# Kernel tuning notes

Measured on AMD Instinct MI355X. Metric: run time of the kernel, lower is better.

## Reference

```python
import jax, jax.numpy as jnp
import numpy as np

G, MAXN, NPG, EPG = 2048, 30, 24, 288   # graphs, dense pad size, real nodes/graph, edges/graph
K, EMB, DH, ATOM_TYPES = 32, 32, 64, 10  # gaussian basis, embed_dim, cfg.gt.dim_hidden, atom types


def setup_inputs() -> dict:
    key = jax.random.key(0)
    ks = jax.random.split(key, 12)
    N = G * NPG
    E = G * EPG
    z = jax.random.randint(ks[0], (N,), 1, ATOM_TYPES).astype(jnp.int32)  # 1..9; 0 = padding idx
    pos = jax.random.normal(ks[1], (N, 3), jnp.float32) * 3.0
    batch_mapping = (jnp.arange(N) // NPG).astype(jnp.int32)
    # radius-graph style edges, endpoints within the same graph (global node ids)
    gidx = jnp.arange(E) // EPG
    src_local = jax.random.randint(ks[2], (E,), 0, NPG)
    dst_local = jax.random.randint(ks[3], (E,), 0, NPG)
    edge_index = jnp.stack([gidx * NPG + src_local, gidx * NPG + dst_local]).astype(jnp.int32)
    atom_emb = (jax.random.normal(ks[4], (ATOM_TYPES, EMB), jnp.float32) * 0.02).at[0].set(0.0)
    W_edge_proj = jax.random.normal(ks[5], (K, EMB), jnp.float32) / np.sqrt(K)
    b_edge_proj = jnp.zeros((EMB,), jnp.float32)
    gbf_means = jax.random.uniform(ks[6], (K,), jnp.float32, minval=0.0, maxval=3.0)
    gbf_stds = jax.random.uniform(ks[7], (K,), jnp.float32, minval=0.1, maxval=2.0)
    gbf_mul = jax.random.normal(ks[8], (ATOM_TYPES * ATOM_TYPES,), jnp.float32)
    gbf_bias = jax.random.normal(ks[9], (ATOM_TYPES * ATOM_TYPES,), jnp.float32)
    W_nodes = jax.random.normal(ks[10], (EMB, DH), jnp.float32) / np.sqrt(EMB)
    b_nodes = jnp.zeros((DH,), jnp.float32)
    W_edges = jax.random.normal(ks[11], (EMB, DH), jnp.float32) / np.sqrt(EMB)
    b_edges = jnp.zeros((DH,), jnp.float32)
    return dict(z=z, pos=pos, batch_mapping=batch_mapping, edge_index=edge_index,
                atom_emb=atom_emb, W_edge_proj=W_edge_proj, b_edge_proj=b_edge_proj,
                gbf_means=gbf_means, gbf_stds=gbf_stds, gbf_mul=gbf_mul, gbf_bias=gbf_bias,
                W_nodes=W_nodes, b_nodes=b_nodes, W_edges=W_edges, b_edges=b_edges)


def reference(z, pos, batch_mapping, edge_index, atom_emb, W_edge_proj, b_edge_proj,
              gbf_means, gbf_stds, gbf_mul, gbf_bias, W_nodes, b_nodes, W_edges, b_edges):
    N = z.shape[0]
    # --- to_dense_batch: local index of each node within its graph ---
    counts = jax.ops.segment_sum(jnp.ones((N,), jnp.int32), batch_mapping, num_segments=G)
    ptr = jnp.concatenate([jnp.zeros((1,), jnp.int32), jnp.cumsum(counts).astype(jnp.int32)])[:-1]
    local = jnp.arange(N, dtype=jnp.int32) - ptr[batch_mapping]
    z_dense = jnp.zeros((G, MAXN), z.dtype).at[batch_mapping, local].set(z)          # [G,30]
    pos_dense = jnp.zeros((G, MAXN, 3), pos.dtype).at[batch_mapping, local].set(pos)  # [G,30,3]
    # --- pairwise distances (safe norm; diagonal is exactly 0) ---
    delta = pos_dense[:, None, :, :] - pos_dense[:, :, None, :]        # [G,30,30,3]: pos_j - pos_i
    sq = jnp.sum(delta * delta, axis=-1)
    dist = jnp.where(sq == 0, 0.0, jnp.sqrt(jnp.where(sq == 0, 1.0, sq)))  # [G,30,30]
    # --- GaussianLayer ---
    edge_type = z_dense[:, :, None] * ATOM_TYPES + z_dense[:, None, :]  # [G,30,30] in [0,100)
    x = gbf_mul[edge_type] * dist + gbf_bias[edge_type]                 # [G,30,30]
    std = jnp.abs(gbf_stds) + 1e-5                                       # [K]
    a = (x[..., None] - gbf_means) / std                                 # [G,30,30,K]
    gbf_feature = jnp.exp(-0.5 * a * a) / (jnp.sqrt(2.0 * jnp.pi) * std)
    # --- mask padded target nodes, reduce over neighbors ---
    pad = (z_dense == 0)
    edge_features = jnp.where(pad[:, None, :, None], 0.0, gbf_feature)   # [G,30,30,K]
    graph_node_feature = atom_emb[z_dense] + edge_features.sum(axis=2) @ W_edge_proj + b_edge_proj  # [G,30,EMB]
    # --- gather real nodes back to flat order (== graph_node_feature[batch_mask]) ---
    node_flat = graph_node_feature[batch_mapping, local]                 # [N,EMB]
    # --- per-edge gather: edge_index rows swapped, global->local via ptr ---
    ei = edge_index[::-1]                                                # [[1,0],:]
    ebm = batch_mapping[ei[0]]
    sl = ei[0] - ptr[ebm]
    dl = ei[1] - ptr[ebm]
    edge_sel = edge_features[ebm, sl, dl, :]                             # [E,K]
    node_feat = node_flat @ W_nodes + b_nodes                            # [N,DH]
    edge_feat = edge_sel @ W_edges + b_edges                             # [E,DH]
    return node_feat, edge_feat
```

## Files before the change

### kernel.cpp

```cpp
#include <hip/hip_runtime.h>
#include <math.h>

static constexpr int GG   = 2048;
static constexpr int NPG  = 24;
static constexpr int EPG  = 288;
static constexpr int NN   = GG * NPG;
static constexpr int EE   = GG * EPG;
static constexpr int DHc  = 64;
static constexpr int NODE_OUT_FLOATS = NN * DHc;
static constexpr int EPB  = 256;
static constexpr int EDGE_BLOCKS = EE / EPB;
static constexpr float INV_SQRT_2PI = 0.3989422804014327f;

typedef __attribute__((ext_vector_type(8))) short bf16x8;
typedef __attribute__((ext_vector_type(4))) float f32x4;

static __device__ __forceinline__ short f2bf(float x) {
  union { float f; unsigned u; } v; v.f = x;
  unsigned r = (v.u + 0x7FFFu + ((v.u >> 16) & 1u)) >> 16;
  return (short)r;
}

struct NodeS {
  float x[576];
  float ns[768];
  float gnf[768];
  float wep[1024];
  float wn[2048];
  float mean[32], inv[32], scale[32];
  float bep[32];
  float bn[64];
  float emb[320];
  float pos[72];
  float mul[100], bias[100];
  int   zz[24];
};
struct EdgeS {
  unsigned char afrag[16 * 1024];
  unsigned char bfrag[4 * 64 * 16];
  float mean[32];
  float inv[32];
  float be[64];
  float mul[100], bias[100];
};
union alignas(16) SMem { NodeS n; EdgeS e; };

__global__ __launch_bounds__(256) void gps_fused_kernel(
    const int*   __restrict__ z,
    const float* __restrict__ pos,
    const int*   __restrict__ ei,
    const float* __restrict__ atom_emb,
    const float* __restrict__ Wep,
    const float* __restrict__ bep,
    const float* __restrict__ means,
    const float* __restrict__ stds,
    const float* __restrict__ gmul,
    const float* __restrict__ gbias,
    const float* __restrict__ Wn,
    const float* __restrict__ bn,
    const float* __restrict__ We,
    const float* __restrict__ be,
    float*       __restrict__ out)
{
  __shared__ SMem sm;
  const int t = threadIdx.x;

  if (blockIdx.x < EDGE_BLOCKS) {
    const int b = blockIdx.x;

    if (t < 32) {
      float sd = fabsf(stds[t]) + 1e-5f;
      sm.e.mean[t] = means[t];
      sm.e.inv[t]  = 1.0f / sd;
    }
    if (t < 64)  sm.e.be[t] = be[t];
    if (t < 100) { sm.e.mul[t] = gmul[t]; sm.e.bias[t] = gbias[t]; }
    {
      const int nt = t >> 6, l = t & 63;
      const int n  = nt * 16 + (l & 15);
      const int k0 = (l >> 4) * 8;
      bf16x8 pk;
#pragma unroll
      for (int j = 0; j < 8; j++) {
        int k = k0 + j;
        float sd = fabsf(stds[k]) + 1e-5f;
        pk[j] = f2bf(We[k * 64 + n] * (INV_SQRT_2PI / sd));
      }
      *(bf16x8*)(sm.e.bfrag + (nt * 64 + l) * 16) = pk;
    }
    __syncthreads();

    {
      const int eg = b * EPB + t;
      const int s = ei[eg], d = ei[EE + eg];
      float dx = pos[d * 3 + 0] - pos[s * 3 + 0];
      float dy = pos[d * 3 + 1] - pos[s * 3 + 1];
      float dz = pos[d * 3 + 2] - pos[s * 3 + 2];
      float dist = sqrtf(dx * dx + dy * dy + dz * dz);
      const int et = z[d] * 10 + z[s];
      const float x = fmaf(sm.e.mul[et], dist, sm.e.bias[et]);

      const int tile = t >> 4, m = t & 15;
      unsigned char* abase = sm.e.afrag + tile * 1024 + m * 16;
      const float4* m4 = (const float4*)sm.e.mean;
      const float4* v4 = (const float4*)sm.e.inv;
#pragma unroll
      for (int q = 0; q < 4; q++) {
        float4 mv0 = m4[q * 2],     vv0 = v4[q * 2];
        float4 mv1 = m4[q * 2 + 1], vv1 = v4[q * 2 + 1];
        float a;
        bf16x8 pk;
        a = (x - mv0.x) * vv0.x; pk[0] = f2bf(__expf(-0.5f * a * a));
        a = (x - mv0.y) * vv0.y; pk[1] = f2bf(__expf(-0.5f * a * a));
        a = (x - mv0.z) * vv0.z; pk[2] = f2bf(__expf(-0.5f * a * a));
        a = (x - mv0.w) * vv0.w; pk[3] = f2bf(__expf(-0.5f * a * a));
        a = (x - mv1.x) * vv1.x; pk[4] = f2bf(__expf(-0.5f * a * a));
        a = (x - mv1.y) * vv1.y; pk[5] = f2bf(__expf(-0.5f * a * a));
        a = (x - mv1.z) * vv1.z; pk[6] = f2bf(__expf(-0.5f * a * a));
        a = (x - mv1.w) * vv1.w; pk[7] = f2bf(__expf(-0.5f * a * a));
        *(bf16x8*)(abase + 16 * 16 * q) = pk;
      }
    }
    __syncthreads();

    {
      const int wv = t >> 6, lane = t & 63;
      const int col = lane & 15, rq = lane >> 4;
      bf16x8 bfr0 = *(const bf16x8*)(sm.e.bfrag + (0 * 64 + lane) * 16);
      bf16x8 bfr1 = *(const bf16x8*)(sm.e.bfrag + (1 * 64 + lane) * 16);
      bf16x8 bfr2 = *(const bf16x8*)(sm.e.bfrag + (2 * 64 + lane) * 16);
      bf16x8 bfr3 = *(const bf16x8*)(sm.e.bfrag + (3 * 64 + lane) * 16);
      float bev0 = sm.e.be[ 0 + col];
      float bev1 = sm.e.be[16 + col];
      float bev2 = sm.e.be[32 + col];
      float bev3 = sm.e.be[48 + col];
#pragma unroll
      for (int it = 0; it < 4; it++) {
        const int tile = wv + it * 4;
        bf16x8 afr = *(const bf16x8*)(sm.e.afrag + tile * 1024 + lane * 16);
        f32x4 c0 = {0.f, 0.f, 0.f, 0.f}, c1 = c0, c2 = c0, c3 = c0;
        c0 = __builtin_amdgcn_mfma_f32_16x16x32_bf16(afr, bfr0, c0, 0, 0, 0);
        c1 = __builtin_amdgcn_mfma_f32_16x16x32_bf16(afr, bfr1, c1, 0, 0, 0);
        c2 = __builtin_amdgcn_mfma_f32_16x16x32_bf16(afr, bfr2, c2, 0, 0, 0);
        c3 = __builtin_amdgcn_mfma_f32_16x16x32_bf16(afr, bfr3, c3, 0, 0, 0);
        float* ob = out + NODE_OUT_FLOATS
                  + ((size_t)(b * EPB + tile * 16 + rq * 4)) * DHc + col;
#pragma unroll
        for (int r = 0; r < 4; r++) {
          float* row = ob + (size_t)r * DHc;
          row[ 0] = c0[r] + bev0;
          row[16] = c1[r] + bev1;
          row[32] = c2[r] + bev2;
          row[48] = c3[r] + bev3;
        }
      }
    }
  } else {
    const int g = blockIdx.x - EDGE_BLOCKS;
    if (t < 72) sm.n.pos[t] = pos[g * 72 + t];
    if (t < 24) sm.n.zz[t] = z[g * 24 + t];
    if (t < 32) {
      float sd = fabsf(stds[t]) + 1e-5f;
      sm.n.mean[t]  = means[t];
      sm.n.inv[t]   = 1.0f / sd;
      sm.n.scale[t] = INV_SQRT_2PI / sd;
      sm.n.bep[t]   = bep[t];
    }
    if (t < 64)  sm.n.bn[t] = bn[t];
    if (t < 100) { sm.n.mul[t] = gmul[t]; sm.n.bias[t] = gbias[t]; }
    for (int i = t; i < 320;  i += 256) sm.n.emb[i] = atom_emb[i];
    for (int i = t; i < 1024; i += 256) sm.n.wep[i] = Wep[i];
    for (int i = t; i < 2048; i += 256) sm.n.wn[i]  = Wn[i];
    __syncthreads();

    for (int p = t; p < 576; p += 256) {
      int i = p / 24, j = p - i * 24;
      float dx = sm.n.pos[i * 3 + 0] - sm.n.pos[j * 3 + 0];
      float dy = sm.n.pos[i * 3 + 1] - sm.n.pos[j * 3 + 1];
      float dz = sm.n.pos[i * 3 + 2] - sm.n.pos[j * 3 + 2];
      float dist = sqrtf(dx * dx + dy * dy + dz * dz);
      int et = sm.n.zz[i] * 10 + sm.n.zz[j];
      sm.n.x[p] = fmaf(sm.n.mul[et], dist, sm.n.bias[et]);
    }
    __syncthreads();

    {
      int k = t & 31, i0 = t >> 5;
      float mk = sm.n.mean[k], ik = sm.n.inv[k], sc = sm.n.scale[k];
      for (int i = i0; i < 24; i += 8) {
        const float4* xr = (const float4*)(sm.n.x + i * 24);
        float acc = 0.0f;
#pragma unroll
        for (int q = 0; q < 6; q++) {
          float4 xv = xr[q];
          float a;
          a = (xv.x - mk) * ik; acc += __expf(-0.5f * a * a);
          a = (xv.y - mk) * ik; acc += __expf(-0.5f * a * a);
          a = (xv.z - mk) * ik; acc += __expf(-0.5f * a * a);
          a = (xv.w - mk) * ik; acc += __expf(-0.5f * a * a);
        }
        sm.n.ns[i * 32 + k] = acc * sc;
      }
    }
    __syncthreads();

    {
      int e = t & 31, i0 = t >> 5;
      float wc[32];
#pragma unroll
      for (int k2 = 0; k2 < 32; k2++) wc[k2] = sm.n.wep[k2 * 32 + e];
      for (int i = i0; i < 24; i += 8) {
        float acc = sm.n.emb[sm.n.zz[i] * 32 + e] + sm.n.bep[e];
        const float4* nr = (const float4*)(sm.n.ns + i * 32);
#pragma unroll
        for (int q = 0; q < 8; q++) {
          float4 nv = nr[q];
          acc = fmaf(nv.x, wc[q * 4 + 0], acc);
          acc = fmaf(nv.y, wc[q * 4 + 1], acc);
          acc = fmaf(nv.z, wc[q * 4 + 2], acc);
          acc = fmaf(nv.w, wc[q * 4 + 3], acc);
        }
        sm.n.gnf[i * 32 + e] = acc;
      }
    }
    __syncthreads();

    {
      int h = t & 63, i0 = t >> 6;
      float wc[32];
#pragma unroll
      for (int e2 = 0; e2 < 32; e2++) wc[e2] = sm.n.wn[e2 * 64 + h];
      for (int i = i0; i < 24; i += 4) {
        float acc = sm.n.bn[h];
        const float4* gr = (const float4*)(sm.n.gnf + i * 32);
#pragma unroll
        for (int q = 0; q < 8; q++) {
          float4 gv = gr[q];
          acc = fmaf(gv.x, wc[q * 4 + 0], acc);
          acc = fmaf(gv.y, wc[q * 4 + 1], acc);
          acc = fmaf(gv.z, wc[q * 4 + 2], acc);
          acc = fmaf(gv.w, wc[q * 4 + 3], acc);
        }
        out[((size_t)(g * 24 + i)) * 64 + h] = acc;
      }
    }
  }
}

extern "C" void kernel_launch(void* const* d_in, const int* in_sizes, int n_in,
                              void* d_out, int out_size, void* d_ws, size_t ws_size,
                              hipStream_t stream) {
  const int*   z        = (const int*)d_in[0];
  const float* pos      = (const float*)d_in[1];
  const int*   ei       = (const int*)d_in[3];
  const float* atom_emb = (const float*)d_in[4];
  const float* Wep      = (const float*)d_in[5];
  const float* bep      = (const float*)d_in[6];
  const float* means    = (const float*)d_in[7];
  const float* stds     = (const float*)d_in[8];
  const float* gmul     = (const float*)d_in[9];
  const float* gbias    = (const float*)d_in[10];
  const float* Wn       = (const float*)d_in[11];
  const float* bn       = (const float*)d_in[12];
  const float* We       = (const float*)d_in[13];
  const float* be       = (const float*)d_in[14];
  float* out = (float*)d_out;

  dim3 grid(EDGE_BLOCKS + GG), block(256);
  gps_fused_kernel<<<grid, block, 0, stream>>>(z, pos, ei, atom_emb, Wep, bep,
                                               means, stds, gmul, gbias,
                                               Wn, bn, We, be, out);
}
```

Baseline: 209.7 us.

## Precompute fused weights in setup kernel and batch four graphs per node block

Adds a small setup kernel that folds Wep@Wn (scaled by the gaussian normalisation) into one 32x64 matrix, builds a per-atom-type table of (emb+bep)@Wn+bn, and packs the bf16 edge weight fragments into the workspace. Node blocks now handle four graphs each and do a single 32x64 matvec per node instead of two chained ones. Edge blocks copy prebuilt fragments instead of recomputing them per block. This cuts redundant per-block weight loading and arithmetic, at the cost of an extra kernel launch, a dependency between the two launches, and a different float rounding order.

```diff
diff --git a/kernel.cpp b/kernel.cpp
--- a/kernel.cpp
+++ b/kernel.cpp
@@ -10,7 +10,11 @@
 static constexpr int NODE_OUT_FLOATS = NN * DHc;
 static constexpr int EPB  = 256;
 static constexpr int EDGE_BLOCKS = EE / EPB;
+static constexpr int GPB  = 4;
+static constexpr int NODE_BLOCKS = GG / GPB;
 static constexpr float INV_SQRT_2PI = 0.3989422804014327f;
+
+static constexpr int WS_W2 = 0, WS_T = 2048, WS_BF = 2688;
 
 typedef __attribute__((ext_vector_type(8))) short bf16x8;
 typedef __attribute__((ext_vector_type(4))) float f32x4;
@@ -21,26 +25,76 @@
   return (short)r;
 }
 
+__global__ __launch_bounds__(256) void gps_setup(
+    const float* __restrict__ atom_emb,
+    const float* __restrict__ Wep,
+    const float* __restrict__ bep,
+    const float* __restrict__ stds,
+    const float* __restrict__ Wn,
+    const float* __restrict__ bn,
+    const float* __restrict__ We,
+    float*       __restrict__ ws)
+{
+  __shared__ float l0[1024];
+  __shared__ float l1[2048];
+  __shared__ float sm_small[416];
+  const int t = threadIdx.x;
+
+  if (blockIdx.x == 0) {
+    for (int i = t; i < 1024; i += 256) l0[i] = Wep[i];
+    for (int i = t; i < 2048; i += 256) l1[i] = Wn[i];
+    __syncthreads();
+    for (int o = t; o < 2048; o += 256) {
+      int k = o >> 6, h = o & 63;
+      float acc = 0.f;
+#pragma unroll
+      for (int e = 0; e < 32; e++) acc = fmaf(l0[k * 32 + e], l1[e * 64 + h], acc);
+      float sd = fabsf(stds[k]) + 1e-5f;
+      ws[WS_W2 + o] = acc * (INV_SQRT_2PI / sd);
+    }
+  } else if (blockIdx.x == 1) {
+    for (int i = t; i < 2048; i += 256) l1[i] = Wn[i];
+    for (int i = t; i < 320;  i += 256) sm_small[i] = atom_emb[i];
+    if (t < 32) sm_small[320 + t] = bep[t];
+    if (t < 64) sm_small[352 + t] = bn[t];
+    __syncthreads();
+    for (int o = t; o < 640; o += 256) {
+      int zt = o >> 6, h = o & 63;
+      float acc = sm_small[352 + h];
+#pragma unroll
+      for (int e = 0; e < 32; e++)
+        acc = fmaf(sm_small[zt * 32 + e] + sm_small[320 + e], l1[e * 64 + h], acc);
+      ws[WS_T + o] = acc;
+    }
+  } else {
+    const int nt = t >> 6, l = t & 63;
+    const int n  = nt * 16 + (l & 15);
+    const int k0 = (l >> 4) * 8;
+    bf16x8 pk;
+#pragma unroll
+    for (int j = 0; j < 8; j++) {
+      int k = k0 + j;
+      float sd = fabsf(stds[k]) + 1e-5f;
+      pk[j] = f2bf(We[k * 64 + n] * (INV_SQRT_2PI / sd));
+    }
+    *(bf16x8*)((char*)ws + (size_t)WS_BF * 4 + t * 16) = pk;
+  }
+}
+
 struct NodeS {
-  float x[576];
-  float ns[768];
-  float gnf[768];
-  float wep[1024];
-  float wn[2048];
-  float mean[32], inv[32], scale[32];
-  float bep[32];
-  float bn[64];
-  float emb[320];
-  float pos[72];
+  float x[GPB * 576];
+  float ns[GPB * 768];
+  float w2[2048];
+  float tt[640];
+  float mean[32], inv[32];
+  float pos[GPB * 72];
   float mul[100], bias[100];
-  int   zz[24];
+  int   zz[GPB * 24];
 };
 struct EdgeS {
   unsigned char afrag[16 * 1024];
-  unsigned char bfrag[4 * 64 * 16];
-  float mean[32];
-  float inv[32];
-  float be[64];
+  unsigned char bfrag[4096];
+  float mean[32], inv[32], be[64];
   float mul[100], bias[100];
 };
 union alignas(16) SMem { NodeS n; EdgeS e; };
@@ -49,25 +103,92 @@
     const int*   __restrict__ z,
     const float* __restrict__ pos,
     const int*   __restrict__ ei,
-    const float* __restrict__ atom_emb,
-    const float* __restrict__ Wep,
-    const float* __restrict__ bep,
     const float* __restrict__ means,
     const float* __restrict__ stds,
     const float* __restrict__ gmul,
     const float* __restrict__ gbias,
-    const float* __restrict__ Wn,
-    const float* __restrict__ bn,
-    const float* __restrict__ We,
     const float* __restrict__ be,
+    const float* __restrict__ ws,
     float*       __restrict__ out)
 {
   __shared__ SMem sm;
   const int t = threadIdx.x;
 
-  if (blockIdx.x < EDGE_BLOCKS) {
-    const int b = blockIdx.x;
-
+  if (blockIdx.x < NODE_BLOCKS) {
+    const int g0 = blockIdx.x * GPB;
+    for (int i = t; i < GPB * 72; i += 256) sm.n.pos[i] = pos[g0 * 72 + i];
+    if (t < GPB * 24) sm.n.zz[t] = z[g0 * 24 + t];
+    if (t < 32) {
+      float sd = fabsf(stds[t]) + 1e-5f;
+      sm.n.mean[t] = means[t];
+      sm.n.inv[t]  = 1.0f / sd;
+    }
+    if (t < 100) { sm.n.mul[t] = gmul[t]; sm.n.bias[t] = gbias[t]; }
+    {
+      const float4* w4 = (const float4*)(ws + WS_W2);
+      float4* d4 = (float4*)sm.n.w2;
+      d4[t] = w4[t];
+      d4[t + 256] = w4[t + 256];
+      const float4* t4 = (const float4*)(ws + WS_T);
+      if (t < 160) ((float4*)sm.n.tt)[t] = t4[t];
+    }
+    __syncthreads();
+
+    for (int p = t; p < GPB * 576; p += 256) {
+      int g2 = p / 576, r = p - g2 * 576;
+      int i = r / 24, j = r - i * 24;
+      const float* pb = sm.n.pos + g2 * 72;
+      float dx = pb[i * 3 + 0] - pb[j * 3 + 0];
+      float dy = pb[i * 3 + 1] - pb[j * 3 + 1];
+      float dz = pb[i * 3 + 2] - pb[j * 3 + 2];
+      float dist = sqrtf(dx * dx + dy * dy + dz * dz);
+      int et = sm.n.zz[g2 * 24 + i] * 10 + sm.n.zz[g2 * 24 + j];
+      sm.n.x[p] = fmaf(sm.n.mul[et], dist, sm.n.bias[et]);
+    }
+    __syncthreads();
+
+    {
+      int k = t & 31, row0 = t >> 5;
+      float mk = sm.n.mean[k], ik = sm.n.inv[k];
+      for (int row = row0; row < GPB * 24; row += 8) {
+        const float4* xr = (const float4*)(sm.n.x + row * 24);
+        float acc = 0.0f;
+#pragma unroll
+        for (int q = 0; q < 6; q++) {
+          float4 xv = xr[q];
+          float a;
+          a = (xv.x - mk) * ik; acc += __expf(-0.5f * a * a);
+          a = (xv.y - mk) * ik; acc += __expf(-0.5f * a * a);
+          a = (xv.z - mk) * ik; acc += __expf(-0.5f * a * a);
+          a = (xv.w - mk) * ik; acc += __expf(-0.5f * a * a);
+        }
+        sm.n.ns[row * 32 + k] = acc;
+      }
+    }
+    __syncthreads();
+
+    {
+      int h = t & 63, r0 = t >> 6;
+      float wc[32];
+#pragma unroll
+      for (int k2 = 0; k2 < 32; k2++) wc[k2] = sm.n.w2[k2 * 64 + h];
+      for (int row = r0; row < GPB * 24; row += 4) {
+        int zv = sm.n.zz[row];
+        float acc = sm.n.tt[zv * 64 + h];
+        const float4* nr = (const float4*)(sm.n.ns + row * 32);
+#pragma unroll
+        for (int q = 0; q < 8; q++) {
+          float4 nv = nr[q];
+          acc = fmaf(nv.x, wc[q * 4 + 0], acc);
+          acc = fmaf(nv.y, wc[q * 4 + 1], acc);
+          acc = fmaf(nv.z, wc[q * 4 + 2], acc);
+          acc = fmaf(nv.w, wc[q * 4 + 3], acc);
+        }
+        out[((size_t)(g0 * 24 + row)) * 64 + h] = acc;
+      }
+    }
+  } else {
+    const int b = blockIdx.x - NODE_BLOCKS;
     if (t < 32) {
       float sd = fabsf(stds[t]) + 1e-5f;
       sm.e.mean[t] = means[t];
@@ -75,19 +196,7 @@
     }
     if (t < 64)  sm.e.be[t] = be[t];
     if (t < 100) { sm.e.mul[t] = gmul[t]; sm.e.bias[t] = gbias[t]; }
-    {
-      const int nt = t >> 6, l = t & 63;
-      const int n  = nt * 16 + (l & 15);
-      const int k0 = (l >> 4) * 8;
-      bf16x8 pk;
-#pragma unroll
-      for (int j = 0; j < 8; j++) {
-        int k = k0 + j;
-        float sd = fabsf(stds[k]) + 1e-5f;
-        pk[j] = f2bf(We[k * 64 + n] * (INV_SQRT_2PI / sd));
-      }
-      *(bf16x8*)(sm.e.bfrag + (nt * 64 + l) * 16) = pk;
-    }
+    ((float4*)sm.e.bfrag)[t] = ((const float4*)((const char*)ws + (size_t)WS_BF * 4))[t];
     __syncthreads();
 
     {
@@ -153,95 +262,6 @@
           row[32] = c2[r] + bev2;
           row[48] = c3[r] + bev3;
         }
-      }
-    }
-  } else {
-    const int g = blockIdx.x - EDGE_BLOCKS;
-    if (t < 72) sm.n.pos[t] = pos[g * 72 + t];
-    if (t < 24) sm.n.zz[t] = z[g * 24 + t];
-    if (t < 32) {
-      float sd = fabsf(stds[t]) + 1e-5f;
-      sm.n.mean[t]  = means[t];
-      sm.n.inv[t]   = 1.0f / sd;
-      sm.n.scale[t] = INV_SQRT_2PI / sd;
-      sm.n.bep[t]   = bep[t];
-    }
-    if (t < 64)  sm.n.bn[t] = bn[t];
-    if (t < 100) { sm.n.mul[t] = gmul[t]; sm.n.bias[t] = gbias[t]; }
-    for (int i = t; i < 320;  i += 256) sm.n.emb[i] = atom_emb[i];
-    for (int i = t; i < 1024; i += 256) sm.n.wep[i] = Wep[i];
-    for (int i = t; i < 2048; i += 256) sm.n.wn[i]  = Wn[i];
-    __syncthreads();
-
-    for (int p = t; p < 576; p += 256) {
-      int i = p / 24, j = p - i * 24;
-      float dx = sm.n.pos[i * 3 + 0] - sm.n.pos[j * 3 + 0];
-      float dy = sm.n.pos[i * 3 + 1] - sm.n.pos[j * 3 + 1];
-      float dz = sm.n.pos[i * 3 + 2] - sm.n.pos[j * 3 + 2];
-      float dist = sqrtf(dx * dx + dy * dy + dz * dz);
-      int et = sm.n.zz[i] * 10 + sm.n.zz[j];
-      sm.n.x[p] = fmaf(sm.n.mul[et], dist, sm.n.bias[et]);
-    }
-    __syncthreads();
-
-    {
-      int k = t & 31, i0 = t >> 5;
-      float mk = sm.n.mean[k], ik = sm.n.inv[k], sc = sm.n.scale[k];
-      for (int i = i0; i < 24; i += 8) {
-        const float4* xr = (const float4*)(sm.n.x + i * 24);
-        float acc = 0.0f;
-#pragma unroll
-        for (int q = 0; q < 6; q++) {
-          float4 xv = xr[q];
-          float a;
-          a = (xv.x - mk) * ik; acc += __expf(-0.5f * a * a);
-          a = (xv.y - mk) * ik; acc += __expf(-0.5f * a * a);
-          a = (xv.z - mk) * ik; acc += __expf(-0.5f * a * a);
-          a = (xv.w - mk) * ik; acc += __expf(-0.5f * a * a);
-        }
-        sm.n.ns[i * 32 + k] = acc * sc;
-      }
-    }
-    __syncthreads();
-
-    {
-      int e = t & 31, i0 = t >> 5;
-      float wc[32];
-#pragma unroll
-      for (int k2 = 0; k2 < 32; k2++) wc[k2] = sm.n.wep[k2 * 32 + e];
-      for (int i = i0; i < 24; i += 8) {
-        float acc = sm.n.emb[sm.n.zz[i] * 32 + e] + sm.n.bep[e];
-        const float4* nr = (const float4*)(sm.n.ns + i * 32);
-#pragma unroll
-        for (int q = 0; q < 8; q++) {
-          float4 nv = nr[q];
-          acc = fmaf(nv.x, wc[q * 4 + 0], acc);
-          acc = fmaf(nv.y, wc[q * 4 + 1], acc);
-          acc = fmaf(nv.z, wc[q * 4 + 2], acc);
-          acc = fmaf(nv.w, wc[q * 4 + 3], acc);
-        }
-        sm.n.gnf[i * 32 + e] = acc;
-      }
-    }
-    __syncthreads();
-
-    {
-      int h = t & 63, i0 = t >> 6;
-      float wc[32];
-#pragma unroll
-      for (int e2 = 0; e2 < 32; e2++) wc[e2] = sm.n.wn[e2 * 64 + h];
-      for (int i = i0; i < 24; i += 4) {
-        float acc = sm.n.bn[h];
-        const float4* gr = (const float4*)(sm.n.gnf + i * 32);
-#pragma unroll
-        for (int q = 0; q < 8; q++) {
-          float4 gv = gr[q];
-          acc = fmaf(gv.x, wc[q * 4 + 0], acc);
-          acc = fmaf(gv.y, wc[q * 4 + 1], acc);
-          acc = fmaf(gv.z, wc[q * 4 + 2], acc);
-          acc = fmaf(gv.w, wc[q * 4 + 3], acc);
-        }
-        out[((size_t)(g * 24 + i)) * 64 + h] = acc;
       }
     }
   }
@@ -265,9 +285,10 @@
   const float* We       = (const float*)d_in[13];
   const float* be       = (const float*)d_in[14];
   float* out = (float*)d_out;
-
-  dim3 grid(EDGE_BLOCKS + GG), block(256);
-  gps_fused_kernel<<<grid, block, 0, stream>>>(z, pos, ei, atom_emb, Wep, bep,
-                                               means, stds, gmul, gbias,
-                                               Wn, bn, We, be, out);
-}
+  float* ws  = (float*)d_ws;
+
+  gps_setup<<<dim3(3), dim3(256), 0, stream>>>(atom_emb, Wep, bep, stds, Wn, bn, We, ws);
+  dim3 grid(NODE_BLOCKS + EDGE_BLOCKS), block(256);
+  gps_fused_kernel<<<grid, block, 0, stream>>>(z, pos, ei, means, stds, gmul, gbias,
+                                               be, ws, out);
+}
```

After: 214.1 us. 2.1% more time.
